# Kernel optimization log

Hardware: AMD Instinct MI355X
Metric: run time of the kernel (lower is better)

## Reference

```python
import jax, jax.numpy as jnp
import numpy as np

SEQ, IN, HID = 8192, 1024, 1024

def setup_inputs() -> dict:
    key = jax.random.key(0)
    k0, k1, k2, k3, k4 = jax.random.split(key, 5)
    s = 1.0 / np.sqrt(HID)  # PyTorch GRU default init scale
    return {
        "inp":  jax.random.normal(k0, (SEQ, IN), jnp.float32),
        "W_ih": jax.random.uniform(k1, (3 * HID, IN), jnp.float32, -s, s),
        "W_hh": jax.random.uniform(k2, (3 * HID, HID), jnp.float32, -s, s),
        "b_ih": jax.random.uniform(k3, (3 * HID,), jnp.float32, -s, s),
        "b_hh": jax.random.uniform(k4, (3 * HID,), jnp.float32, -s, s),
    }

def reference(inp, W_ih, W_hh, b_ih, b_hh):
    # Precompute input-side gate projections for all timesteps in one GEMM: [S, 3H]
    gx = inp @ W_ih.T + b_ih
    h0 = jnp.zeros((HID,), inp.dtype)

    def step(h, gx_t):
        gh = W_hh @ h + b_hh           # [3H]
        xr, xz, xn = jnp.split(gx_t, 3)
        hr, hz, hn = jnp.split(gh, 3)
        r = jax.nn.sigmoid(xr + hr)
        z = jax.nn.sigmoid(xz + hz)
        n = jnp.tanh(xn + r * hn)      # PyTorch GRU: r gates the hidden candidate term
        h_new = (1.0 - z) * n + z * h
        return h_new, h_new

    _, outs = jax.lax.scan(step, h0, gx)  # outs: [S, H], matches torch loop output
    return outs
```

## Files before the change

### kernel.cpp

```cpp
#include <hip/hip_runtime.h>

#define SEQ  8192
#define HID  1024
#define NBLK 64
#define WPB  16
#define TPB  (WPB * 64)
#define KCH  (HID / 64)

#define SLOT_WORDS (2 * HID)

__device__ __forceinline__ float sigmoidf_fast(float a) {
    return 1.0f / (1.0f + __expf(-a));
}
__device__ __forceinline__ float tanhf_fast(float a) {
    float t = fabsf(a);
    float e = __expf(-2.0f * t);
    float r = (1.0f - e) / (1.0f + e);
    return copysignf(r, a);
}

__global__ __launch_bounds__(TPB, 4) void gru_persistent(
    const float* __restrict__ inp,
    const float* __restrict__ Wih,
    const float* __restrict__ Whh,
    const float* __restrict__ bih,
    const float* __restrict__ bhh,
    float* __restrict__ out,
    unsigned long long* __restrict__ slots)
{
    __shared__ float hbuf[2][HID];
    const int tid  = threadIdx.x;
    const int wave = tid >> 6;
    const int lane = tid & 63;
    const int j    = blockIdx.x * WPB + wave;
    const int sl   = (wave << 6) | lane;

    float wr[KCH], wz[KCH], wn[KCH];
    {
        const float* Wr = Whh + (size_t)j * HID;
        const float* Wz = Whh + (size_t)(HID + j) * HID;
        const float* Wn = Whh + (size_t)(2 * HID + j) * HID;
#pragma unroll
        for (int k = 0; k < KCH; ++k) {
            wr[k] = Wr[lane + 64 * k];
            wz[k] = Wz[lane + 64 * k];
            wn[k] = Wn[lane + 64 * k];
        }
    }
    const float bxr = bih[j], bxz = bih[HID + j], bxn = bih[2 * HID + j];
    const float bhr = bhh[j], bhz = bhh[HID + j], bhn = bhh[2 * HID + j];
    const float* Ur = Wih + (size_t)j * HID;
    const float* Uz = Wih + (size_t)(HID + j) * HID;
    const float* Un = Wih + (size_t)(2 * HID + j) * HID;

    hbuf[0][tid] = 0.0f;
    __syncthreads();

    float xr = 0.0f, xz = 0.0f, xn = 0.0f;
    {
        const float* x = inp;
#pragma unroll
        for (int k = 0; k < KCH; ++k) {
            float xv = x[lane + 64 * k];
            xr = fmaf(Ur[lane + 64 * k], xv, xr);
            xz = fmaf(Uz[lane + 64 * k], xv, xz);
            xn = fmaf(Un[lane + 64 * k], xv, xn);
        }
#pragma unroll
        for (int m = 32; m >= 1; m >>= 1) {
            xr += __shfl_xor(xr, m, 64);
            xz += __shfl_xor(xz, m, 64);
            xn += __shfl_xor(xn, m, 64);
        }
        xr += bxr; xz += bxz; xn += bxn;
    }

    for (int t = 1; t <= SEQ; ++t) {
        const float* hb = hbuf[(t - 1) & 1];
        float hr = 0.0f, hz = 0.0f, hn = 0.0f;
#pragma unroll
        for (int k = 0; k < KCH; ++k) {
            float hv = hb[lane + 64 * k];
            hr = fmaf(wr[k], hv, hr);
            hz = fmaf(wz[k], hv, hz);
            hn = fmaf(wn[k], hv, hn);
        }
#pragma unroll
        for (int m = 32; m >= 1; m >>= 1) {
            hr += __shfl_xor(hr, m, 64);
            hz += __shfl_xor(hz, m, 64);
            hn += __shfl_xor(hn, m, 64);
        }
        hr += bhr; hz += bhz; hn += bhn;

        const float hprev = hb[j];
        const float r = sigmoidf_fast(xr + hr);
        const float z = sigmoidf_fast(xz + hz);
        const float n = tanhf_fast(xn + r * hn);
        const float hnew = (1.0f - z) * n + z * hprev;

        if (lane == 0) {
            unsigned long long pub = ((unsigned long long)(unsigned)t << 32)
                                   | (unsigned long long)__float_as_uint(hnew);
            __hip_atomic_store(slots + (t & 1) * HID + j, pub,
                               __ATOMIC_RELAXED, __HIP_MEMORY_SCOPE_AGENT);
            __builtin_nontemporal_store(hnew, out + (size_t)(t - 1) * HID + j);
        }

        if (t < SEQ) {
            {
                const float* x = inp + (size_t)t * HID;
                xr = 0.0f; xz = 0.0f; xn = 0.0f;
#pragma unroll
                for (int k = 0; k < KCH; ++k) {
                    float xv = x[lane + 64 * k];
                    xr = fmaf(Ur[lane + 64 * k], xv, xr);
                    xz = fmaf(Uz[lane + 64 * k], xv, xz);
                    xn = fmaf(Un[lane + 64 * k], xv, xn);
                }
#pragma unroll
                for (int m = 32; m >= 1; m >>= 1) {
                    xr += __shfl_xor(xr, m, 64);
                    xz += __shfl_xor(xz, m, 64);
                    xn += __shfl_xor(xn, m, 64);
                }
                xr += bxr; xz += bxz; xn += bxn;
            }

            const unsigned long long* rd = slots + (t & 1) * HID;
            const unsigned expect = (unsigned)t;
            for (;;) {
                unsigned long long wv = __hip_atomic_load(
                    rd + sl, __ATOMIC_RELAXED, __HIP_MEMORY_SCOPE_AGENT);
                if (__all((unsigned)(wv >> 32) == expect)) {
                    hbuf[t & 1][sl] = __uint_as_float((unsigned)(wv & 0xffffffffu));
                    break;
                }
                __builtin_amdgcn_s_sleep(1);
            }
        }
        __syncthreads();
    }
}

extern "C" void kernel_launch(void* const* d_in, const int* in_sizes, int n_in,
                              void* d_out, int out_size, void* d_ws, size_t ws_size,
                              hipStream_t stream) {
    const float* inp = (const float*)d_in[0];
    const float* Wih = (const float*)d_in[1];
    const float* Whh = (const float*)d_in[2];
    const float* bih = (const float*)d_in[3];
    const float* bhh = (const float*)d_in[4];
    float* out = (float*)d_out;
    unsigned long long* slots = (unsigned long long*)d_ws;

    hipMemsetAsync(slots, 0, SLOT_WORDS * sizeof(unsigned long long), stream);

    gru_persistent<<<dim3(NBLK), dim3(TPB), 0, stream>>>(
        inp, Wih, Whh, bih, bhh, out, slots);
}
```

Before: 68.31 ms.

## Replace per-slot tagged polling with grouped arrival counters before reading hidden state

Each block now publishes its hidden values, waits for those stores to complete, synchronises, and then increments one of eight padded arrival counters. Only wave 0 polls the counters until all blocks have arrived, then loads the full hidden vector with tag checks and fills shared memory. This aims to cut the global polling traffic that came from every wave spinning on its own tagged slots. It adds an extra block barrier, a vmcnt wait and a counter atomic to each step, and shared-memory filling now falls to a single wave.

```diff
diff --git a/kernel.cpp b/kernel.cpp
--- a/kernel.cpp
+++ b/kernel.cpp
@@ -8,6 +8,9 @@
 #define KCH  (HID / 64)
 
 #define SLOT_WORDS (2 * HID)
+#define NCTR       8
+#define CTR_STRIDE 64
+#define CTR_U32OFF 4096
 
 __device__ __forceinline__ float sigmoidf_fast(float a) {
     return 1.0f / (1.0f + __expf(-a));
@@ -26,14 +29,15 @@
     const float* __restrict__ bih,
     const float* __restrict__ bhh,
     float* __restrict__ out,
-    unsigned long long* __restrict__ slots)
+    unsigned long long* __restrict__ slots,
+    unsigned* __restrict__ ctr)
 {
     __shared__ float hbuf[2][HID];
     const int tid  = threadIdx.x;
     const int wave = tid >> 6;
     const int lane = tid & 63;
     const int j    = blockIdx.x * WPB + wave;
-    const int sl   = (wave << 6) | lane;
+    const int grp  = blockIdx.x & (NCTR - 1);
 
     float wr[KCH], wz[KCH], wn[KCH];
     {
@@ -99,15 +103,23 @@
         const float n = tanhf_fast(xn + r * hn);
         const float hnew = (1.0f - z) * n + z * hprev;
 
-        if (lane == 0) {
-            unsigned long long pub = ((unsigned long long)(unsigned)t << 32)
-                                   | (unsigned long long)__float_as_uint(hnew);
-            __hip_atomic_store(slots + (t & 1) * HID + j, pub,
-                               __ATOMIC_RELAXED, __HIP_MEMORY_SCOPE_AGENT);
-            __builtin_nontemporal_store(hnew, out + (size_t)(t - 1) * HID + j);
-        }
+        if (t < SEQ) {
+            if (lane == 0) {
+                unsigned long long pub = ((unsigned long long)(unsigned)t << 32)
+                                       | (unsigned long long)__float_as_uint(hnew);
+                __hip_atomic_store(slots + (t & 1) * HID + j, pub,
+                                   __ATOMIC_RELAXED, __HIP_MEMORY_SCOPE_AGENT);
+            }
+            asm volatile("s_waitcnt vmcnt(0)" ::: "memory");
+            __syncthreads();
+            if (tid == 0) {
+                __hip_atomic_fetch_add(ctr + grp * CTR_STRIDE, 1u,
+                                       __ATOMIC_RELAXED, __HIP_MEMORY_SCOPE_AGENT);
+            }
+            if (lane == 0) {
+                __builtin_nontemporal_store(hnew, out + (size_t)(t - 1) * HID + j);
+            }
 
-        if (t < SEQ) {
             {
                 const float* x = inp + (size_t)t * HID;
                 xr = 0.0f; xz = 0.0f; xn = 0.0f;
@@ -127,16 +139,38 @@
                 xr += bxr; xz += bxz; xn += bxn;
             }
 
-            const unsigned long long* rd = slots + (t & 1) * HID;
-            const unsigned expect = (unsigned)t;
-            for (;;) {
-                unsigned long long wv = __hip_atomic_load(
-                    rd + sl, __ATOMIC_RELAXED, __HIP_MEMORY_SCOPE_AGENT);
-                if (__all((unsigned)(wv >> 32) == expect)) {
-                    hbuf[t & 1][sl] = __uint_as_float((unsigned)(wv & 0xffffffffu));
-                    break;
+            if (wave == 0) {
+                const unsigned tgt = (unsigned)(t * (NBLK / NCTR));
+                for (;;) {
+                    unsigned c = __hip_atomic_load(
+                        ctr + (lane & (NCTR - 1)) * CTR_STRIDE,
+                        __ATOMIC_RELAXED, __HIP_MEMORY_SCOPE_AGENT);
+                    if (__all(c >= tgt)) break;
+                    __builtin_amdgcn_s_sleep(1);
                 }
-                __builtin_amdgcn_s_sleep(1);
+                const unsigned long long* rdp = slots + (t & 1) * HID;
+                const unsigned expect = (unsigned)t;
+                for (;;) {
+                    float v[KCH];
+                    bool ok = true;
+#pragma unroll
+                    for (int k = 0; k < KCH; ++k) {
+                        unsigned long long wv = __hip_atomic_load(
+                            rdp + lane + 64 * k, __ATOMIC_RELAXED, __HIP_MEMORY_SCOPE_AGENT);
+                        ok &= ((unsigned)(wv >> 32) == expect);
+                        v[k] = __uint_as_float((unsigned)(wv & 0xffffffffu));
+                    }
+                    if (__all(ok)) {
+#pragma unroll
+                        for (int k = 0; k < KCH; ++k) hbuf[t & 1][lane + 64 * k] = v[k];
+                        break;
+                    }
+                    __builtin_amdgcn_s_sleep(1);
+                }
+            }
+        } else {
+            if (lane == 0) {
+                __builtin_nontemporal_store(hnew, out + (size_t)(t - 1) * HID + j);
             }
         }
         __syncthreads();
@@ -153,9 +187,10 @@
     const float* bhh = (const float*)d_in[4];
     float* out = (float*)d_out;
     unsigned long long* slots = (unsigned long long*)d_ws;
+    unsigned* ctr = (unsigned*)d_ws + CTR_U32OFF;
 
-    hipMemsetAsync(slots, 0, SLOT_WORDS * sizeof(unsigned long long), stream);
+    hipMemsetAsync(d_ws, 0, 32768, stream);
 
     gru_persistent<<<dim3(NBLK), dim3(TPB), 0, stream>>>(
-        inp, Wih, Whh, bih, bhh, out, slots);
+        inp, Wih, Whh, bih, bhh, out, slots, ctr);
 }
```

After: 69.77 ms. 2.1% more time.

## Coalesce per-block h publish and poll cross-block sync from a single wave

Applied to the files above, without the earlier changes.

Each wave's new hidden value is gathered into shared memory, and one wave then publishes the block's 16 values in a single coalesced store. Waiting is reduced to wave 0: it first polls one sentinel slot per block, then reads all 1024 tagged values and copies them into shared memory. The aim is less polling traffic to the L2/atomic path, fewer waves spinning, and fewer scattered publish stores. The cost is an extra __syncthreads per step and a serialized 16-load fetch done by one wave instead of spread across all waves.

```diff
diff --git a/kernel.cpp b/kernel.cpp
--- a/kernel.cpp
+++ b/kernel.cpp
@@ -29,11 +29,11 @@
     unsigned long long* __restrict__ slots)
 {
     __shared__ float hbuf[2][HID];
+    __shared__ unsigned long long hg[WPB];
     const int tid  = threadIdx.x;
     const int wave = tid >> 6;
     const int lane = tid & 63;
     const int j    = blockIdx.x * WPB + wave;
-    const int sl   = (wave << 6) | lane;
 
     float wr[KCH], wz[KCH], wn[KCH];
     {
@@ -100,14 +100,21 @@
         const float hnew = (1.0f - z) * n + z * hprev;
 
         if (lane == 0) {
-            unsigned long long pub = ((unsigned long long)(unsigned)t << 32)
-                                   | (unsigned long long)__float_as_uint(hnew);
-            __hip_atomic_store(slots + (t & 1) * HID + j, pub,
-                               __ATOMIC_RELAXED, __HIP_MEMORY_SCOPE_AGENT);
             __builtin_nontemporal_store(hnew, out + (size_t)(t - 1) * HID + j);
         }
 
         if (t < SEQ) {
+            if (lane == 0) {
+                hg[wave] = ((unsigned long long)(unsigned)t << 32)
+                         | (unsigned long long)__float_as_uint(hnew);
+            }
+            __syncthreads();
+
+            if (wave == 0 && lane < WPB) {
+                __hip_atomic_store(slots + (t & 1) * HID + blockIdx.x * WPB + lane,
+                                   hg[lane], __ATOMIC_RELAXED, __HIP_MEMORY_SCOPE_AGENT);
+            }
+
             {
                 const float* x = inp + (size_t)t * HID;
                 xr = 0.0f; xz = 0.0f; xn = 0.0f;
@@ -127,16 +134,32 @@
                 xr += bxr; xz += bxz; xn += bxn;
             }
 
-            const unsigned long long* rd = slots + (t & 1) * HID;
-            const unsigned expect = (unsigned)t;
-            for (;;) {
-                unsigned long long wv = __hip_atomic_load(
-                    rd + sl, __ATOMIC_RELAXED, __HIP_MEMORY_SCOPE_AGENT);
-                if (__all((unsigned)(wv >> 32) == expect)) {
-                    hbuf[t & 1][sl] = __uint_as_float((unsigned)(wv & 0xffffffffu));
-                    break;
+            if (wave == 0) {
+                const unsigned long long* rd = slots + (t & 1) * HID;
+                const unsigned expect = (unsigned)t;
+                for (;;) {
+                    unsigned long long w0 = __hip_atomic_load(
+                        rd + lane * WPB, __ATOMIC_RELAXED, __HIP_MEMORY_SCOPE_AGENT);
+                    if (__all((unsigned)(w0 >> 32) == expect)) break;
+                    __builtin_amdgcn_s_sleep(2);
                 }
-                __builtin_amdgcn_s_sleep(1);
+                for (;;) {
+                    float v[KCH];
+                    bool ok = true;
+#pragma unroll
+                    for (int k = 0; k < KCH; ++k) {
+                        unsigned long long wv = __hip_atomic_load(
+                            rd + lane + 64 * k, __ATOMIC_RELAXED, __HIP_MEMORY_SCOPE_AGENT);
+                        ok &= ((unsigned)(wv >> 32) == expect);
+                        v[k] = __uint_as_float((unsigned)(wv & 0xffffffffu));
+                    }
+                    if (__all(ok)) {
+#pragma unroll
+                        for (int k = 0; k < KCH; ++k) hbuf[t & 1][lane + 64 * k] = v[k];
+                        break;
+                    }
+                    __builtin_amdgcn_s_sleep(1);
+                }
             }
         }
         __syncthreads();
```

Result: faster. 64.54 ms (-5.5%).
